# Kernel optimization log

Hardware: AMD Instinct MI355X
Metric: run time of the kernel (lower is better)

Reference implementation:

```python
import jax, jax.numpy as jnp
import numpy as np

B, N, IN, E, H, F = 64, 256, 128, 256, 8, 1024


def setup_inputs() -> dict:
    key = jax.random.key(0)
    ks = jax.random.split(key, 16)
    x = jax.random.normal(ks[0], (B, N, IN), jnp.float32)
    adj = (jax.random.uniform(ks[1], (B, N, N)) < 0.1).astype(jnp.float32)
    adj = jnp.maximum(adj, adj.transpose(0, 2, 1))  # symmetric 0/1 adjacency
    mask = jax.random.randint(ks[2], (B, N), 0, 2).astype(jnp.float32)
    dist = jax.random.normal(ks[3], (B, N, N), jnp.float32)

    def lin(k, i, o):
        return (jax.random.normal(k, (i, o), jnp.float32) / np.sqrt(i)).astype(jnp.float32)

    return dict(
        x=x, adj=adj, mask=mask, dist=dist,
        W1=lin(ks[4], IN, E), b1=jnp.zeros((E,), jnp.float32),
        W2=lin(ks[5], E, E), b2=jnp.zeros((E,), jnp.float32),
        W3=lin(ks[6], E, E), b3=jnp.zeros((E,), jnp.float32),
        ln1_g=jnp.ones((E,), jnp.float32), ln1_b=jnp.zeros((E,), jnp.float32),
        Wq=lin(ks[7], E, H * E), Wk=lin(ks[8], E, H * E), Wv=lin(ks[9], E, H * E),
        Wo=lin(ks[10], H * E, E), bo=jnp.zeros((E,), jnp.float32),
        ln2_g=jnp.ones((E,), jnp.float32), ln2_b=jnp.zeros((E,), jnp.float32),
        Wf1=lin(ks[11], E, F), bf1=jnp.zeros((F,), jnp.float32),
        Wf2=lin(ks[12], F, E), bf2=jnp.zeros((E,), jnp.float32),
    )


def _layernorm(x, g, b):
    m = x.mean(-1, keepdims=True)
    v = ((x - m) ** 2).mean(-1, keepdims=True)
    return (x - m) * jax.lax.rsqrt(v + 1e-5) * g + b


def reference(x, adj, mask, dist, W1, b1, W2, b2, W3, b3, ln1_g, ln1_b,
              Wq, Wk, Wv, Wo, bo, ln2_g, ln2_b, Wf1, bf1, Wf2, bf2):
    # --- DenseGCNConv normalization (add self-loops, sym-normalize) ---
    eye = jnp.eye(N, dtype=adj.dtype)
    A = adj * (1.0 - eye) + eye                      # fill_diag(adj, 1)
    dis = jax.lax.rsqrt(jnp.clip(A.sum(-1), 1.0, None))
    An = dis[:, :, None] * A * dis[:, None, :]       # D^-1/2 A D^-1/2, [B,N,N]
    m3 = mask[:, :, None]

    def gcn(h, W, b):
        return (jnp.einsum('bij,bjf->bif', An, h @ W) + b) * m3

    g1 = jax.nn.relu(gcn(x, W1, b1))
    g2 = jax.nn.relu(gcn(g1, W2, b2))
    g3 = jax.nn.relu(gcn(g2, W3, b3))
    gcn_res = g1 + g2 + g3

    # --- masked MHA with distance bias (head dim = E per head) ---
    h = _layernorm(gcn_res, ln1_g, ln1_b)
    mh = mask[:, None, :, None]                      # [B,1,N,1]
    q = (h @ Wq).reshape(B, N, H, E).transpose(0, 2, 1, 3) * mh
    k = (h @ Wk).reshape(B, N, H, E).transpose(0, 2, 1, 3) * mh
    v = (h @ Wv).reshape(B, N, H, E).transpose(0, 2, 1, 3) * mh
    a = jnp.einsum('bhne,bhme->bhnm', q * (E ** -0.5), k) + dist[:, None]
    am = (mask[:, :, None] * mask[:, None, :])[:, None]  # [B,1,N,N]
    a = jnp.where(am == 0, -1e9, a)
    a = jax.nn.softmax(a, axis=-1)
    a = jnp.where(am == 0, 0.0, a)
    y = jnp.einsum('bhnm,bhme->bhne', a, v).transpose(0, 2, 1, 3).reshape(B, N, H * E)
    y = (y @ Wo + bo) * m3
    att = gcn_res + y

    # --- FFN block ---
    f = _layernorm(att, ln2_g, ln2_b)
    f = (jax.nn.gelu(f @ Wf1 + bf1, approximate=False) @ Wf2 + bf2) * m3
    att = att + f
    return gcn_res + att
```

## Files before the change

### kernel.cpp

```cpp
#include <hip/hip_runtime.h>
#include <hip/hip_bf16.h>
#include <cmath>

#define BB 64
#define NNODES 256
#define INF_ 128
#define EE 256
#define HH 8
#define FFN 1024
#define BNROWS 16384

typedef __attribute__((ext_vector_type(8))) short short8;
typedef __attribute__((ext_vector_type(4))) float floatx4;
typedef __attribute__((ext_vector_type(4))) unsigned short ushort4v;

__device__ __forceinline__ float b2f(unsigned short u) {
  union { unsigned u32; float f; } w; w.u32 = ((unsigned)u) << 16; return w.f;
}
__device__ __forceinline__ unsigned short f2b(float f) {
  union { float f; unsigned u32; } w; w.f = f;
  unsigned r = w.u32 + 0x7FFFu + ((w.u32 >> 16) & 1u);
  return (unsigned short)(r >> 16);
}
__device__ __forceinline__ float gelu_f(float x) {
  const float z = 0.7978845608028654f * (x + 0.044715f * x * x * x);
  const float e = __expf(2.0f * z);
  const float th = (e - 1.0f) / (e + 1.0f);
  return 0.5f * x * (1.0f + th);
}

typedef const __attribute__((address_space(1))) void GV;
typedef __attribute__((address_space(3))) void LV;

__device__ __forceinline__ void gl_lds16(const unsigned short* g,
                                         unsigned short* l, int lane) {
#if __has_builtin(__builtin_amdgcn_global_load_lds)
  __builtin_amdgcn_global_load_lds((GV*)g, (LV*)l, 16, 0, 0);
#else
  *(short8*)(l + lane * 8) = *(const short8*)g;
#endif
}

struct PackArgs {
  const float* src[12];
  unsigned short* dst[12];
  int R[12], C[12];
  int start[13];
};

__launch_bounds__(256)
__global__ void pack_kernel(PackArgs a)
{
  __shared__ float tile[32][33];
  const int bid = blockIdx.x;
  int j = 0;
  while (bid >= a.start[j + 1]) j++;
  const int lb = bid - a.start[j];
  const float* src = a.src[j];
  unsigned short* dst = a.dst[j];
  const int R = a.R[j], C = a.C[j];

  if (C == 0) {
    const int i = (lb * 256 + threadIdx.x) * 4;
    if (i >= R) return;
    floatx4 v = *(const floatx4*)(src + i);
    ushort4v o;
    #pragma unroll
    for (int k = 0; k < 4; k++) o[k] = f2b(v[k]);
    *(ushort4v*)(dst + i) = o;
    return;
  }
  const int tpr = C >> 5;
  const int c0 = (lb % tpr) * 32, r0 = (lb / tpr) * 32;
  const int tx = threadIdx.x & 31, ty = threadIdx.x >> 5;
  #pragma unroll
  for (int i = ty; i < 32; i += 8)
    tile[i][tx] = src[(long long)(r0 + i) * C + c0 + tx];
  __syncthreads();
  #pragma unroll
  for (int i = ty; i < 32; i += 8)
    dst[(long long)(c0 + i) * R + r0 + tx] = f2b(tile[tx][i]);
}

__global__ void deg_kernel(const float* __restrict__ adj,
                           float* __restrict__ dis)
{
  const int g = blockIdx.x * 4 + (threadIdx.x >> 6);
  const int lane = threadIdx.x & 63;
  const int i = g & 255;
  floatx4 v = *(const floatx4*)(adj + (long long)g * 256 + lane * 4);
  float s = 0.f;
  #pragma unroll
  for (int jj = 0; jj < 4; jj++) {
    const int j = lane * 4 + jj;
    s += (j == i) ? 1.0f : v[jj];
  }
  #pragma unroll
  for (int off = 32; off > 0; off >>= 1) s += __shfl_xor(s, off);
  if (lane == 0) dis[g] = 1.0f / sqrtf(fmaxf(s, 1.0f));
}

__global__ void an_kernel(const float* __restrict__ adj,
                          const float* __restrict__ dis,
                          unsigned short* __restrict__ An)
{
  const long long base = ((long long)blockIdx.x * 256 + threadIdx.x) * 4;
  const int rowg = (int)(base >> 8);
  const int i = rowg & 255;
  const int brow = rowg & ~255;
  const int j0 = (int)(base & 255);
  const float di = dis[rowg];
  floatx4 v = *(const floatx4*)(adj + base);
  ushort4v o;
  #pragma unroll
  for (int jj = 0; jj < 4; jj++) {
    const int j = j0 + jj;
    const float a = (j == i) ? 1.0f : v[jj];
    o[jj] = f2b(di * dis[brow + j] * a);
  }
  *(ushort4v*)(An + base) = o;
}

__launch_bounds__(512, 4)
__global__ void gemm_kernel(const unsigned short* __restrict__ A, int lda,
                            long long sAo, long long sAi,
                            const unsigned short* __restrict__ Bm, int ldb,
                            long long sBo, long long sBi,
                            void* __restrict__ Cv, int ldc,
                            long long sCo, long long sCi,
                            int K, int zshift, int mode, int flag,
                            const float* __restrict__ aux1,
                            const float* __restrict__ mask,
                            float* __restrict__ gcn,
                            void* __restrict__ aux2)
{
  __shared__ __align__(16) unsigned short sA[16384];
  __shared__ __align__(16) unsigned short sB[16384];

  const int t = threadIdx.x;
  const int z = blockIdx.z;
  const int zi = z & ((1 << zshift) - 1);
  const int zb = z >> zshift;
  const int m0 = blockIdx.x * 128;
  const int n0 = blockIdx.y * 128;
  A  += zb * sAo + zi * sAi;
  Bm += zb * sBo + zi * sBi;
  const long long cbase = zb * sCo + zi * sCi;

  const int lane = t & 63;
  const int w = t >> 6;
  const int wm = w >> 2, wn = w & 3;
  const int lm = lane & 15, qd = lane >> 4;

  floatx4 acc[4][2] = {};

  const int sub = lane >> 4;
  const int qs  = lane & 15;
  const unsigned short* pA[4];
  const unsigned short* pB[4];
  #pragma unroll
  for (int i = 0; i < 4; i++) {
    const int d = w * 4 + i;
    const int r = d * 4 + sub;
    const int co = (qs ^ (r & 7)) * 8;
    pA[i] = A + (long long)(m0 + r) * lda + co;
    pB[i] = Bm + (long long)(n0 + r) * ldb + co;
  }

  for (int kk = 0; kk < K; kk += 128) {
    #pragma unroll
    for (int i = 0; i < 4; i++) {
      gl_lds16(pA[i] + kk, &sA[(w * 4 + i) * 512], lane);
      gl_lds16(pB[i] + kk, &sB[(w * 4 + i) * 512], lane);
    }
    __syncthreads();

    #pragma unroll
    for (int ks = 0; ks < 4; ks++) {
      short8 af[4], bg[2];
      const int q = ks * 4 + qd;
      #pragma unroll
      for (int mi = 0; mi < 4; mi++) {
        const int r = wm * 64 + mi * 16 + lm;
        af[mi] = *(const short8*)&sA[r * 128 + ((q ^ (r & 7)) * 8)];
      }
      #pragma unroll
      for (int ni = 0; ni < 2; ni++) {
        const int r = wn * 32 + ni * 16 + lm;
        bg[ni] = *(const short8*)&sB[r * 128 + ((q ^ (r & 7)) * 8)];
      }
      #pragma unroll
      for (int mi = 0; mi < 4; mi++)
        #pragma unroll
        for (int ni = 0; ni < 2; ni++)
          acc[mi][ni] = __builtin_amdgcn_mfma_f32_16x16x32_bf16(
              af[mi], bg[ni], acc[mi][ni], 0, 0, 0);
    }
    __syncthreads();
  }

  #pragma unroll
  for (int mi = 0; mi < 4; mi++) {
    const int row0 = m0 + wm * 64 + mi * 16 + qd * 4;
    #pragma unroll
    for (int ni = 0; ni < 2; ni++) {
      const int col = n0 + wn * 32 + ni * 16 + lm;
      floatx4 a = acc[mi][ni];
      if (mode == 0) {
        float* Cf = (float*)Cv;
        #pragma unroll
        for (int r = 0; r < 4; r++)
          Cf[cbase + (long long)(row0 + r) * ldc + col] = a[r];
      } else if (mode == 1) {
        unsigned short* Cb = (unsigned short*)Cv;
        #pragma unroll
        for (int r = 0; r < 4; r++)
          Cb[cbase + (long long)(row0 + r) * ldc + col] = f2b(a[r]);
      } else if (mode == 2) {
        float* Cf = (float*)Cv;
        #pragma unroll
        for (int r = 0; r < 4; r++)
          Cf[cbase + (long long)(row0 + r) * ldc + col] += a[r];
      } else if (mode == 3) {
        unsigned short* Cb = (unsigned short*)Cv;
        const float bv = aux1[col];
        #pragma unroll
        for (int r = 0; r < 4; r++)
          Cb[cbase + (long long)(row0 + r) * ldc + col] = f2b(gelu_f(a[r] + bv));
      } else if (mode == 5) {
        const int b = row0 >> 8, n = row0 & 255;
        ushort4v o;
        #pragma unroll
        for (int r = 0; r < 4; r++) o[r] = f2b(a[r]);
        *(ushort4v*)((unsigned short*)Cv + (long long)b * 65536 + col * 256 + n) = o;
      } else if (mode == 8) {
        float* Cf = (float*)Cv;
        const float* attf = (const float*)aux2;
        const float bv = aux1[col];
        #pragma unroll
        for (int r = 0; r < 4; r++) {
          const long long idx = (long long)(row0 + r) * 256 + col;
          Cf[idx] = gcn[idx] + attf[idx] + (a[r] + bv) * mask[row0 + r];
        }
      } else if (mode == 9) {
        const int token = zb * 256 + col;
        const float m = mask[token];
        ushort4v o; floatx4 g;
        #pragma unroll
        for (int r = 0; r < 4; r++) {
          const float v = fmaxf((a[r] + aux1[row0 + r]) * m, 0.f);
          o[r] = f2b(v); g[r] = v;
        }
        *(ushort4v*)((unsigned short*)Cv + (long long)token * 256 + row0) = o;
        float* gp = gcn + (long long)token * 256 + row0;
        if (flag) { floatx4 old = *(const floatx4*)gp; g += old; }
        *(floatx4*)gp = g;
      } else if (mode == 12) {
        float* Cf = (float*)Cv;
        const float bv = aux1[col];
        #pragma unroll
        for (int r = 0; r < 4; r++) {
          const long long idx = (long long)(row0 + r) * 256 + col;
          Cf[idx] = gcn[idx] + (a[r] + bv) * mask[row0 + r];
        }
      } else if (mode == 13) {
        unsigned short* Cb = (unsigned short*)Cv;
        #pragma unroll
        for (int r = 0; r < 4; r++)
          Cb[cbase + (long long)(row0 + r) * ldc + col] = f2b(a[r] * 0.0625f);
      } else {
        if (col < 2048) {
          unsigned short* Cb = (unsigned short*)Cv;
          #pragma unroll
          for (int r = 0; r < 4; r++)
            Cb[(long long)(row0 + r) * 2048 + col] = f2b(a[r]);
        } else {
          const int z2 = (row0 >> 8) * 8 + ((col >> 8) - 8);
          const int e = col & 255, n = row0 & 255;
          ushort4v o;
          #pragma unroll
          for (int r = 0; r < 4; r++) o[r] = f2b(a[r]);
          *(ushort4v*)((unsigned short*)aux2 + (long long)z2 * 65536 + e * 256 + n) = o;
        }
      }
    }
  }
}

__launch_bounds__(512, 4)
__global__ void attn_kernel(unsigned short* __restrict__ QP,
                            const unsigned short* __restrict__ HBF,
                            const unsigned short* __restrict__ VT,
                            const unsigned short* __restrict__ DSTB,
                            const float* __restrict__ mask)
{
  __shared__ __align__(16) unsigned short sP[16896];
  __shared__ __align__(16) unsigned short sKV[16384];
  __shared__ float redm[4][64];
  __shared__ float reds[4][64];

  const int bi = blockIdx.x;
  const int x = bi & 7;
  const int h = (bi >> 3) & 7;
  const int p = (bi >> 6) * 8 + x;
  const int b = p >> 2, mt = p & 3;
  const int m0 = mt * 64;
  const int z = b * 8 + h;

  const int t = threadIdx.x, lane = t & 63, w = t >> 6;
  const int lm = lane & 15, qd = lane >> 4;
  const int wm2 = w >> 2, wn4 = w & 3;

  unsigned short* Qm = QP + ((long long)(b * 256 + m0)) * 2048 + h * 256;
  const unsigned short* Hb = HBF + (long long)b * 65536;
  const unsigned short* Vb = VT + (long long)z * 65536;
  const unsigned short* db = DSTB + (long long)b * 65536 + (long long)m0 * 256;
  const float* maskb = mask + b * 256;

  const int rin2 = lane >> 5, qs32 = lane & 31;
  const int rin8 = lane >> 3, qs8  = lane & 7;

  floatx4 S[2][4];
  #pragma unroll
  for (int mi = 0; mi < 2; mi++)
    #pragma unroll
    for (int ni = 0; ni < 4; ni++) {
      const int col = wn4 * 64 + ni * 16 + lm;
      #pragma unroll
      for (int r = 0; r < 4; r++) {
        const int row = wm2 * 32 + mi * 16 + qd * 4 + r;
        S[mi][ni][r] = b2f(db[row * 256 + col]);
      }
    }

  #pragma unroll
  for (int i = 0; i < 4; i++) {
    const int d = w * 4 + i;
    const int r = d * 2 + rin2;
    gl_lds16(Qm + (long long)r * 2048 + ((qs32 ^ (r & 7)) * 8), &sP[d * 512], lane);
  }
  #pragma unroll
  for (int i = 0; i < 4; i++) {
    const int d = w * 4 + i;
    const int r = d * 8 + rin8;
    gl_lds16(Hb + (long long)r * 256 + ((qs8 ^ (r & 7)) * 8), &sKV[d * 512], lane);
  }
  __syncthreads();

  for (int c = 0; c < 4; c++) {
    __builtin_amdgcn_s_setprio(1);
    #pragma unroll
    for (int ks = 0; ks < 2; ks++) {
      const int ol = ks * 4 + qd;
      short8 af[2], bg[4];
      #pragma unroll
      for (int mi = 0; mi < 2; mi++) {
        const int r = wm2 * 32 + mi * 16 + lm;
        const int q = c * 8 + ol;
        af[mi] = *(const short8*)&sP[r * 256 + ((q ^ (r & 7)) * 8)];
      }
      #pragma unroll
      for (int ni = 0; ni < 4; ni++) {
        const int kk = wn4 * 64 + ni * 16 + lm;
        bg[ni] = *(const short8*)&sKV[kk * 64 + ((ol ^ (kk & 7)) * 8)];
      }
      #pragma unroll
      for (int mi = 0; mi < 2; mi++)
        #pragma unroll
        for (int ni = 0; ni < 4; ni++)
          S[mi][ni] = __builtin_amdgcn_mfma_f32_16x16x32_bf16(
              af[mi], bg[ni], S[mi][ni], 0, 0, 0);
    }
    __builtin_amdgcn_s_setprio(0);
    __syncthreads();
    if (c < 3) {
      #pragma unroll
      for (int i = 0; i < 4; i++) {
        const int d = w * 4 + i;
        const int r = d * 8 + rin8;
        gl_lds16(Hb + (long long)r * 256 + (c + 1) * 64 + ((qs8 ^ (r & 7)) * 8),
                 &sKV[d * 512], lane);
      }
      __syncthreads();
    }
  }

  #pragma unroll
  for (int i = 0; i < 4; i++) {
    const int d = w * 4 + i;
    const int r = d * 8 + rin8;
    gl_lds16(Vb + (long long)r * 256 + ((qs8 ^ (r & 7)) * 8), &sKV[d * 512], lane);
  }

  float mkv[4];
  #pragma unroll
  for (int ni = 0; ni < 4; ni++) mkv[ni] = maskb[wn4 * 64 + ni * 16 + lm];

  float lred[2][4];
  #pragma unroll
  for (int mi = 0; mi < 2; mi++) {
    #pragma unroll
    for (int r = 0; r < 4; r++) {
      const int row = wm2 * 32 + mi * 16 + qd * 4 + r;
      const float mq = maskb[m0 + row];
      float mx = -3e38f;
      #pragma unroll
      for (int ni = 0; ni < 4; ni++) {
        const float v = (mq != 0.f && mkv[ni] != 0.f) ? S[mi][ni][r] : -1e9f;
        S[mi][ni][r] = v;
        mx = fmaxf(mx, v);
      }
      lred[mi][r] = mx;
    }
  }
  #pragma unroll
  for (int off = 1; off < 16; off <<= 1)
    #pragma unroll
    for (int mi = 0; mi < 2; mi++)
      #pragma unroll
      for (int r = 0; r < 4; r++)
        lred[mi][r] = fmaxf(lred[mi][r], __shfl_xor(lred[mi][r], off));
  if (lm == 0)
    #pragma unroll
    for (int mi = 0; mi < 2; mi++)
      #pragma unroll
      for (int r = 0; r < 4; r++)
        redm[wn4][wm2 * 32 + mi * 16 + qd * 4 + r] = lred[mi][r];
  __syncthreads();

  #pragma unroll
  for (int mi = 0; mi < 2; mi++) {
    #pragma unroll
    for (int r = 0; r < 4; r++) {
      const int row = wm2 * 32 + mi * 16 + qd * 4 + r;
      const float gmax = fmaxf(fmaxf(redm[0][row], redm[1][row]),
                               fmaxf(redm[2][row], redm[3][row]));
      float ss = 0.f;
      #pragma unroll
      for (int ni = 0; ni < 4; ni++) {
        const float e = __expf(S[mi][ni][r] - gmax);
        S[mi][ni][r] = e;
        ss += e;
      }
      lred[mi][r] = ss;
    }
  }
  #pragma unroll
  for (int off = 1; off < 16; off <<= 1)
    #pragma unroll
    for (int mi = 0; mi < 2; mi++)
      #pragma unroll
      for (int r = 0; r < 4; r++)
        lred[mi][r] += __shfl_xor(lred[mi][r], off);
  if (lm == 0)
    #pragma unroll
    for (int mi = 0; mi < 2; mi++)
      #pragma unroll
      for (int r = 0; r < 4; r++)
        reds[wn4][wm2 * 32 + mi * 16 + qd * 4 + r] = lred[mi][r];
  __syncthreads();

  #pragma unroll
  for (int mi = 0; mi < 2; mi++)
    #pragma unroll
    for (int r = 0; r < 4; r++) {
      const int row = wm2 * 32 + mi * 16 + qd * 4 + r;
      const float inv = 1.0f / (reds[0][row] + reds[1][row] +
                                reds[2][row] + reds[3][row]);
      #pragma unroll
      for (int ni = 0; ni < 4; ni++) {
        const int kl = ni * 16 + lm;
        const int slot = (kl >> 3) ^ (row & 7);
        sP[wn4 * 4096 + row * 64 + slot * 8 + (kl & 7)] =
            f2b(S[mi][ni][r] * inv);
      }
    }
  __syncthreads();

  floatx4 Y[2][4] = {};
  for (int c = 0; c < 4; c++) {
    __builtin_amdgcn_s_setprio(1);
    #pragma unroll
    for (int ks = 0; ks < 2; ks++) {
      const int ol = ks * 4 + qd;
      short8 af[2], bg[4];
      #pragma unroll
      for (int mi = 0; mi < 2; mi++) {
        const int r = wm2 * 32 + mi * 16 + lm;
        af[mi] = *(const short8*)&sP[c * 4096 + r * 64 + ((ol ^ (r & 7)) * 8)];
      }
      #pragma unroll
      for (int ni = 0; ni < 4; ni++) {
        const int ee = wn4 * 64 + ni * 16 + lm;
        bg[ni] = *(const short8*)&sKV[ee * 64 + ((ol ^ (ee & 7)) * 8)];
      }
      #pragma unroll
      for (int mi = 0; mi < 2; mi++)
        #pragma unroll
        for (int ni = 0; ni < 4; ni++)
          Y[mi][ni] = __builtin_amdgcn_mfma_f32_16x16x32_bf16(
              af[mi], bg[ni], Y[mi][ni], 0, 0, 0);
    }
    __builtin_amdgcn_s_setprio(0);
    __syncthreads();
    if (c < 3) {
      #pragma unroll
      for (int i = 0; i < 4; i++) {
        const int d = w * 4 + i;
        const int r = d * 8 + rin8;
        gl_lds16(Vb + (long long)r * 256 + (c + 1) * 64 + ((qs8 ^ (r & 7)) * 8),
                 &sKV[d * 512], lane);
      }
      __syncthreads();
    }
  }

  #pragma unroll
  for (int mi = 0; mi < 2; mi++)
    #pragma unroll
    for (int ni = 0; ni < 4; ni++) {
      const int col = wn4 * 64 + ni * 16 + lm;
      #pragma unroll
      for (int r = 0; r < 4; r++) {
        const int rl = wm2 * 32 + mi * 16 + qd * 4 + r;
        sP[rl * 264 + col] = f2b(Y[mi][ni][r]);
      }
    }
  __syncthreads();
  #pragma unroll
  for (int it = 0; it < 4; it++) {
    const int idx = it * 512 + t;
    const int row = idx >> 5, u = idx & 31;
    short8 v = *(const short8*)&sP[row * 264 + u * 8];
    *(short8*)(Qm + (long long)row * 2048 + u * 8) = v;
  }
}

__global__ void ln_kernel(const float* __restrict__ X,
                          const float* __restrict__ gam,
                          const float* __restrict__ bet,
                          unsigned short* __restrict__ out)
{
  const int g = blockIdx.x * 4 + (threadIdx.x >> 6);
  const int lane = threadIdx.x & 63;
  floatx4 v = *(const floatx4*)(X + (long long)g * 256 + lane * 4);
  float s = v[0] + v[1] + v[2] + v[3];
  float sq = v[0]*v[0] + v[1]*v[1] + v[2]*v[2] + v[3]*v[3];
  #pragma unroll
  for (int off = 32; off > 0; off >>= 1) {
    s  += __shfl_xor(s, off);
    sq += __shfl_xor(sq, off);
  }
  const float mean = s * (1.0f / 256.0f);
  const float var = sq * (1.0f / 256.0f) - mean * mean;
  const float rs = 1.0f / sqrtf(var + 1e-5f);
  ushort4v o;
  #pragma unroll
  for (int jj = 0; jj < 4; jj++) {
    const int c = lane * 4 + jj;
    o[jj] = f2b((v[jj] - mean) * rs * gam[c] + bet[c]);
  }
  *(ushort4v*)(out + (long long)g * 256 + lane * 4) = o;
}

static inline void launch_gemm(hipStream_t st, int M, int N, int batch,
    const void* A, int lda, long long sAo, long long sAi,
    const void* B, int ldb, long long sBo, long long sBi,
    void* C, int ldc, long long sCo, long long sCi,
    int K, int zshift, int mode, int flag,
    const float* aux1, const float* mask, float* gcn, void* aux2)
{
  dim3 grid(M / 128, N / 128, batch), blk(512);
  gemm_kernel<<<grid, blk, 0, st>>>(
      (const unsigned short*)A, lda, sAo, sAi,
      (const unsigned short*)B, ldb, sBo, sBi,
      C, ldc, sCo, sCi, K, zshift, mode, flag, aux1, mask, gcn, aux2);
}

extern "C" void kernel_launch(void* const* d_in, const int* in_sizes, int n_in,
                              void* d_out, int out_size, void* d_ws, size_t ws_size,
                              hipStream_t stream)
{
  (void)in_sizes; (void)n_in; (void)out_size;
  const float* x    = (const float*)d_in[0];
  const float* adj  = (const float*)d_in[1];
  const float* mask = (const float*)d_in[2];
  const float* dist = (const float*)d_in[3];
  const float* W1   = (const float*)d_in[4];
  const float* b1   = (const float*)d_in[5];
  const float* W2   = (const float*)d_in[6];
  const float* b2   = (const float*)d_in[7];
  const float* W3   = (const float*)d_in[8];
  const float* b3   = (const float*)d_in[9];
  const float* ln1g = (const float*)d_in[10];
  const float* ln1b = (const float*)d_in[11];
  const float* Wq   = (const float*)d_in[12];
  const float* Wk   = (const float*)d_in[13];
  const float* Wv   = (const float*)d_in[14];
  const float* Wo   = (const float*)d_in[15];
  const float* bo   = (const float*)d_in[16];
  const float* ln2g = (const float*)d_in[17];
  const float* ln2b = (const float*)d_in[18];
  const float* Wf1  = (const float*)d_in[19];
  const float* bf1  = (const float*)d_in[20];
  const float* Wf2  = (const float*)d_in[21];
  const float* bf2  = (const float*)d_in[22];

  char* w = (char*)d_ws;
  auto alloc = [&](size_t sz) { void* p = (void*)w; w += sz; return p; };
  unsigned short* W1T   = (unsigned short*)alloc(65536);
  unsigned short* W2T   = (unsigned short*)alloc(131072);
  unsigned short* W3T   = (unsigned short*)alloc(131072);
  unsigned short* ABH   = (unsigned short*)alloc(1048576);
  unsigned short* WVT   = (unsigned short*)alloc(1048576);
  unsigned short* WOT   = (unsigned short*)alloc(1048576);
  unsigned short* WF1T  = (unsigned short*)alloc(524288);
  unsigned short* WF2T  = (unsigned short*)alloc(524288);
  unsigned short* WQb   = (unsigned short*)alloc(1048576);
  unsigned short* WKb   = (unsigned short*)alloc(1048576);
  unsigned short* XBF   = (unsigned short*)alloc(4194304);
  unsigned short* DSTB  = (unsigned short*)alloc(8388608);
  float*          GCN   = (float*)         alloc(16777216);
  float*          U     = (float*)         alloc(16777216);
  unsigned short* HBF   = (unsigned short*)alloc(8388608);
  float*          DIS   = (float*)         alloc(65536);
  char* scratch = (char*)alloc(134217728);
  if ((size_t)(w - (char*)d_ws) > ws_size) return;
  unsigned short* AN  = (unsigned short*)scratch;
  unsigned short* TT  = (unsigned short*)(scratch + 8388608);
  unsigned short* GBF = (unsigned short*)(scratch + 16777216);
  unsigned short* QPB = (unsigned short*)scratch;
  unsigned short* VT  = (unsigned short*)(scratch + 67108864);
  unsigned short* FFB = (unsigned short*)scratch;

  PackArgs pa;
  const float* srcs[11] = {W1, W2, W3, Wv, Wo, Wf1, Wf2, x, Wq, Wk, dist};
  unsigned short* dsts[11] = {W1T, W2T, W3T, WVT, WOT, WF1T, WF2T, XBF, WQb, WKb, DSTB};
  const int Rs[11] = {128, 256, 256, 256, 2048, 256, 1024,
                      BNROWS * INF_, EE * HH * EE, EE * HH * EE, BB * 65536};
  const int Cs[11] = {256, 256, 256, 2048, 256, 1024, 256, 0, 0, 0, 0};
  const int sts[12] = {0, 32, 96, 160, 672, 1184, 1440, 1696, 3744, 4256, 4768, 8864};
  for (int j = 0; j < 11; j++) {
    pa.src[j] = srcs[j]; pa.dst[j] = dsts[j]; pa.R[j] = Rs[j]; pa.C[j] = Cs[j];
  }
  for (int j = 0; j < 12; j++) pa.start[j] = sts[j];
  pack_kernel<<<8864, 256, 0, stream>>>(pa);

  deg_kernel<<<4096, 256, 0, stream>>>(adj, DIS);
  an_kernel<<<4096, 256, 0, stream>>>(adj, DIS, AN);

  launch_gemm(stream, 256, 256, 8, WKb, 2048, 256, 0, WQb, 2048, 256, 0,
              ABH, 256, 65536, 0, 256, 0, 13, 0, nullptr, nullptr, nullptr, nullptr);

  launch_gemm(stream, BNROWS, EE, 1, XBF, 128, 0,0, W1T, 128, 0,0,
              TT, 256, 0,0, 128, 0, 5, 0, nullptr, nullptr, nullptr, nullptr);
  launch_gemm(stream, 256, 256, BB, TT, 256, 65536,0, AN, 256, 65536,0,
              GBF, 256, 0,0, 256, 0, 9, 0, b1, mask, GCN, nullptr);
  launch_gemm(stream, BNROWS, EE, 1, GBF, 256, 0,0, W2T, 256, 0,0,
              TT, 256, 0,0, 256, 0, 5, 0, nullptr, nullptr, nullptr, nullptr);
  launch_gemm(stream, 256, 256, BB, TT, 256, 65536,0, AN, 256, 65536,0,
              GBF, 256, 0,0, 256, 0, 9, 1, b2, mask, GCN, nullptr);
  launch_gemm(stream, BNROWS, EE, 1, GBF, 256, 0,0, W3T, 256, 0,0,
              TT, 256, 0,0, 256, 0, 5, 0, nullptr, nullptr, nullptr, nullptr);
  launch_gemm(stream, 256, 256, BB, TT, 256, 65536,0, AN, 256, 65536,0,
              GBF, 256, 0,0, 256, 0, 9, 1, b3, mask, GCN, nullptr);

  ln_kernel<<<4096, 256, 0, stream>>>(GCN, ln1g, ln1b, HBF);

  launch_gemm(stream, BNROWS, 4096, 1, HBF, 256, 0,0, ABH, 256, 0,0,
              QPB, 2048, 0,0, 256, 0, 15, 0, nullptr, nullptr, nullptr, VT);
  attn_kernel<<<2048, 512, 0, stream>>>(QPB, HBF, VT, DSTB, mask);
  launch_gemm(stream, BNROWS, EE, 1, QPB, 2048, 0,0, WOT, 2048, 0,0,
              U, 256, 0,0, 2048, 0, 12, 0, bo, mask, GCN, nullptr);

  ln_kernel<<<4096, 256, 0, stream>>>(U, ln2g, ln2b, HBF);
  launch_gemm(stream, BNROWS, FFN, 1, HBF, 256, 0,0, WF1T, 256, 0,0,
              FFB, 1024, 0,0, 256, 0, 3, 0, bf1, nullptr, nullptr, nullptr);
  launch_gemm(stream, BNROWS, EE, 1, FFB, 1024, 0,0, WF2T, 1024, 0,0,
              d_out, 256, 0,0, 1024, 0, 8, 0, bf2, mask, GCN, U);
}
```

Baseline: 467.4 us.

## Fuse query projection into attention kernel and double-buffer K/V staging

The separate GEMM that produced the projected queries (h·Wq·Wk^T folded into ABH) is removed. The projection is now computed inside the attention kernel from the layer-normed rows, so the pre-attention GEMM only produces V (N halves from 4096 to 2048 columns). The attention kernel gains a unified double-buffered staging pipeline using explicit vmcnt waits and raw barriers in place of __syncthreads. The aim is to avoid writing and re-reading the large projected-query buffer and to overlap global-to-LDS loads with MFMA work. In exchange, each block recomputes its 64x256x256 projection and relies on hand-managed wait counts.

```diff
diff --git a/kernel.cpp b/kernel.cpp
--- a/kernel.cpp
+++ b/kernel.cpp
@@ -40,6 +40,13 @@
   *(short8*)(l + lane * 8) = *(const short8*)g;
 #endif
 }
+
+#define VMW2() asm volatile("s_waitcnt vmcnt(2)" ::: "memory")
+#define VMW0() asm volatile("s_waitcnt vmcnt(0)" ::: "memory")
+#define LGW0() asm volatile("s_waitcnt lgkmcnt(0)" ::: "memory")
+#define MBAR() do { asm volatile("" ::: "memory"); \
+                    __builtin_amdgcn_s_barrier(); \
+                    asm volatile("" ::: "memory"); } while (0)
 
 struct PackArgs {
   const float* src[12];
@@ -269,19 +276,12 @@
         for (int r = 0; r < 4; r++)
           Cb[cbase + (long long)(row0 + r) * ldc + col] = f2b(a[r] * 0.0625f);
       } else {
-        if (col < 2048) {
-          unsigned short* Cb = (unsigned short*)Cv;
-          #pragma unroll
-          for (int r = 0; r < 4; r++)
-            Cb[(long long)(row0 + r) * 2048 + col] = f2b(a[r]);
-        } else {
-          const int z2 = (row0 >> 8) * 8 + ((col >> 8) - 8);
-          const int e = col & 255, n = row0 & 255;
-          ushort4v o;
-          #pragma unroll
-          for (int r = 0; r < 4; r++) o[r] = f2b(a[r]);
-          *(ushort4v*)((unsigned short*)aux2 + (long long)z2 * 65536 + e * 256 + n) = o;
-        }
+        const int z2 = (row0 >> 8) * 8 + (col >> 8);
+        const int e = col & 255, n = row0 & 255;
+        ushort4v o;
+        #pragma unroll
+        for (int r = 0; r < 4; r++) o[r] = f2b(a[r]);
+        *(ushort4v*)((unsigned short*)aux2 + (long long)z2 * 65536 + e * 256 + n) = o;
       }
     }
   }
@@ -290,12 +290,13 @@
 __launch_bounds__(512, 4)
 __global__ void attn_kernel(unsigned short* __restrict__ QP,
                             const unsigned short* __restrict__ HBF,
+                            const unsigned short* __restrict__ ABH,
                             const unsigned short* __restrict__ VT,
                             const unsigned short* __restrict__ DSTB,
                             const float* __restrict__ mask)
 {
-  __shared__ __align__(16) unsigned short sP[16896];
-  __shared__ __align__(16) unsigned short sKV[16384];
+  __shared__ __align__(16) unsigned short sR0[16896];
+  __shared__ __align__(16) unsigned short sS[16384];
   __shared__ float redm[4][64];
   __shared__ float reds[4][64];
 
@@ -311,15 +312,14 @@
   const int lm = lane & 15, qd = lane >> 4;
   const int wm2 = w >> 2, wn4 = w & 3;
 
-  unsigned short* Qm = QP + ((long long)(b * 256 + m0)) * 2048 + h * 256;
+  unsigned short* Ym = QP + ((long long)(b * 256 + m0)) * 2048 + h * 256;
   const unsigned short* Hb = HBF + (long long)b * 65536;
+  const unsigned short* Hq = Hb + (long long)m0 * 256;
+  const unsigned short* Ah = ABH + (long long)h * 65536;
   const unsigned short* Vb = VT + (long long)z * 65536;
   const unsigned short* db = DSTB + (long long)b * 65536 + (long long)m0 * 256;
   const float* maskb = mask + b * 256;
 
-  const int rin2 = lane >> 5, qs32 = lane & 31;
-  const int rin8 = lane >> 3, qs8  = lane & 7;
-
   floatx4 S[2][4];
   #pragma unroll
   for (int mi = 0; mi < 2; mi++)
@@ -333,63 +333,111 @@
       }
     }
 
-  #pragma unroll
-  for (int i = 0; i < 4; i++) {
-    const int d = w * 4 + i;
-    const int r = d * 2 + rin2;
-    gl_lds16(Qm + (long long)r * 2048 + ((qs32 ^ (r & 7)) * 8), &sP[d * 512], lane);
-  }
-  #pragma unroll
-  for (int i = 0; i < 4; i++) {
-    const int d = w * 4 + i;
-    const int r = d * 8 + rin8;
-    gl_lds16(Hb + (long long)r * 256 + ((qs8 ^ (r & 7)) * 8), &sKV[d * 512], lane);
-  }
-  __syncthreads();
-
-  for (int c = 0; c < 4; c++) {
+  int eoff0, eoff1;
+  {
+    const int rA = lane >> 2, sl = lane & 3;
+    const int r0 = (w * 2 + 0) * 16 + rA;
+    const int r1 = (w * 2 + 1) * 16 + rA;
+    eoff0 = r0 * 256 + ((sl ^ ((r0 >> 1) & 3)) * 8);
+    eoff1 = r1 * 256 + ((sl ^ ((r1 >> 1) & 3)) * 8);
+  }
+  const int ld0 = (w * 2 + 0) * 512;
+  const int ld1 = (w * 2 + 1) * 512;
+
+  auto STAGE = [&](int c) {
+    const unsigned short* bp =
+        (c < 8 ? Ah : (c < 16 ? Hb : Vb)) + (c & 7) * 32;
+    const int bb = (c & 1) * 8192;
+    gl_lds16(bp + eoff0, &sS[bb + ld0], lane);
+    gl_lds16(bp + eoff1, &sS[bb + ld1], lane);
+  };
+
+  {
+    const int rin2 = lane >> 5, qs32 = lane & 31;
+    #pragma unroll
+    for (int i = 0; i < 4; i++) {
+      const int d = w * 4 + i;
+      const int r = d * 2 + rin2;
+      gl_lds16(Hq + (long long)r * 256 + ((qs32 ^ (r & 7)) * 8),
+               &sR0[d * 512], lane);
+    }
+  }
+  STAGE(0); STAGE(1);
+  VMW2();
+  MBAR();
+
+  floatx4 accq[2][4] = {};
+  #pragma unroll
+  for (int c = 0; c < 8; c++) {
     __builtin_amdgcn_s_setprio(1);
-    #pragma unroll
-    for (int ks = 0; ks < 2; ks++) {
-      const int ol = ks * 4 + qd;
-      short8 af[2], bg[4];
-      #pragma unroll
-      for (int mi = 0; mi < 2; mi++) {
-        const int r = wm2 * 32 + mi * 16 + lm;
-        const int q = c * 8 + ol;
-        af[mi] = *(const short8*)&sP[r * 256 + ((q ^ (r & 7)) * 8)];
-      }
+    short8 af[2], bg[4];
+    #pragma unroll
+    for (int mi = 0; mi < 2; mi++) {
+      const int r = wm2 * 32 + mi * 16 + lm;
+      const int q = c * 4 + qd;
+      af[mi] = *(const short8*)&sR0[r * 256 + ((q ^ (r & 7)) * 8)];
+    }
+    const int bb = (c & 1) * 8192;
+    #pragma unroll
+    for (int ni = 0; ni < 4; ni++) {
+      const int rr = wn4 * 64 + ni * 16 + lm;
+      bg[ni] = *(const short8*)&sS[bb + rr * 32 + ((qd ^ ((rr >> 1) & 3)) * 8)];
+    }
+    #pragma unroll
+    for (int mi = 0; mi < 2; mi++)
+      #pragma unroll
+      for (int ni = 0; ni < 4; ni++)
+        accq[mi][ni] = __builtin_amdgcn_mfma_f32_16x16x32_bf16(
+            af[mi], bg[ni], accq[mi][ni], 0, 0, 0);
+    __builtin_amdgcn_s_setprio(0);
+    MBAR();
+    STAGE(c + 2);
+    VMW2();
+    MBAR();
+  }
+
+  #pragma unroll
+  for (int mi = 0; mi < 2; mi++)
+    #pragma unroll
+    for (int rr = 0; rr < 4; rr++) {
+      const int row = wm2 * 32 + mi * 16 + qd * 4 + rr;
       #pragma unroll
       for (int ni = 0; ni < 4; ni++) {
-        const int kk = wn4 * 64 + ni * 16 + lm;
-        bg[ni] = *(const short8*)&sKV[kk * 64 + ((ol ^ (kk & 7)) * 8)];
-      }
-      #pragma unroll
-      for (int mi = 0; mi < 2; mi++)
-        #pragma unroll
-        for (int ni = 0; ni < 4; ni++)
-          S[mi][ni] = __builtin_amdgcn_mfma_f32_16x16x32_bf16(
-              af[mi], bg[ni], S[mi][ni], 0, 0, 0);
-    }
+        const int col = wn4 * 64 + ni * 16 + lm;
+        const int o = col >> 3;
+        sR0[row * 256 + ((o ^ (row & 7)) * 8) + (col & 7)] = f2b(accq[mi][ni][rr]);
+      }
+    }
+  LGW0();
+  MBAR();
+
+  #pragma unroll
+  for (int c = 8; c < 16; c++) {
+    __builtin_amdgcn_s_setprio(1);
+    short8 af[2], bg[4];
+    #pragma unroll
+    for (int mi = 0; mi < 2; mi++) {
+      const int r = wm2 * 32 + mi * 16 + lm;
+      const int q = (c - 8) * 4 + qd;
+      af[mi] = *(const short8*)&sR0[r * 256 + ((q ^ (r & 7)) * 8)];
+    }
+    const int bb = (c & 1) * 8192;
+    #pragma unroll
+    for (int ni = 0; ni < 4; ni++) {
+      const int rr = wn4 * 64 + ni * 16 + lm;
+      bg[ni] = *(const short8*)&sS[bb + rr * 32 + ((qd ^ ((rr >> 1) & 3)) * 8)];
+    }
+    #pragma unroll
+    for (int mi = 0; mi < 2; mi++)
+      #pragma unroll
+      for (int ni = 0; ni < 4; ni++)
+        S[mi][ni] = __builtin_amdgcn_mfma_f32_16x16x32_bf16(
+            af[mi], bg[ni], S[mi][ni], 0, 0, 0);
     __builtin_amdgcn_s_setprio(0);
-    __syncthreads();
-    if (c < 3) {
-      #pragma unroll
-      for (int i = 0; i < 4; i++) {
-        const int d = w * 4 + i;
-        const int r = d * 8 + rin8;
-        gl_lds16(Hb + (long long)r * 256 + (c + 1) * 64 + ((qs8 ^ (r & 7)) * 8),
-                 &sKV[d * 512], lane);
-      }
-      __syncthreads();
-    }
-  }
-
-  #pragma unroll
-  for (int i = 0; i < 4; i++) {
-    const int d = w * 4 + i;
-    const int r = d * 8 + rin8;
-    gl_lds16(Vb + (long long)r * 256 + ((qs8 ^ (r & 7)) * 8), &sKV[d * 512], lane);
+    MBAR();
+    STAGE(c + 2);
+    VMW2();
+    MBAR();
   }
 
   float mkv[4];
@@ -426,7 +474,8 @@
       #pragma unroll
       for (int r = 0; r < 4; r++)
         redm[wn4][wm2 * 32 + mi * 16 + qd * 4 + r] = lred[mi][r];
-  __syncthreads();
+  LGW0();
+  MBAR();
 
   #pragma unroll
   for (int mi = 0; mi < 2; mi++) {
@@ -458,7 +507,8 @@
       #pragma unroll
       for (int r = 0; r < 4; r++)
         reds[wn4][wm2 * 32 + mi * 16 + qd * 4 + r] = lred[mi][r];
-  __syncthreads();
+  LGW0();
+  MBAR();
 
   #pragma unroll
   for (int mi = 0; mi < 2; mi++)
@@ -471,47 +521,46 @@
       for (int ni = 0; ni < 4; ni++) {
         const int kl = ni * 16 + lm;
         const int slot = (kl >> 3) ^ (row & 7);
-        sP[wn4 * 4096 + row * 64 + slot * 8 + (kl & 7)] =
+        sR0[wn4 * 4096 + row * 64 + slot * 8 + (kl & 7)] =
             f2b(S[mi][ni][r] * inv);
       }
     }
-  __syncthreads();
+  LGW0();
+  MBAR();
 
   floatx4 Y[2][4] = {};
-  for (int c = 0; c < 4; c++) {
+  #pragma unroll
+  for (int c = 16; c < 24; c++) {
     __builtin_amdgcn_s_setprio(1);
-    #pragma unroll
-    for (int ks = 0; ks < 2; ks++) {
-      const int ol = ks * 4 + qd;
-      short8 af[2], bg[4];
-      #pragma unroll
-      for (int mi = 0; mi < 2; mi++) {
-        const int r = wm2 * 32 + mi * 16 + lm;
-        af[mi] = *(const short8*)&sP[c * 4096 + r * 64 + ((ol ^ (r & 7)) * 8)];
-      }
-      #pragma unroll
-      for (int ni = 0; ni < 4; ni++) {
-        const int ee = wn4 * 64 + ni * 16 + lm;
-        bg[ni] = *(const short8*)&sKV[ee * 64 + ((ol ^ (ee & 7)) * 8)];
-      }
-      #pragma unroll
-      for (int mi = 0; mi < 2; mi++)
-        #pragma unroll
-        for (int ni = 0; ni < 4; ni++)
-          Y[mi][ni] = __builtin_amdgcn_mfma_f32_16x16x32_bf16(
-              af[mi], bg[ni], Y[mi][ni], 0, 0, 0);
-    }
+    const int pp = (c - 16) >> 1;
+    const int op = ((c - 16) & 1) * 4 + qd;
+    short8 af[2], bg[4];
+    #pragma unroll
+    for (int mi = 0; mi < 2; mi++) {
+      const int r = wm2 * 32 + mi * 16 + lm;
+      af[mi] = *(const short8*)&sR0[pp * 4096 + r * 64 + ((op ^ (r & 7)) * 8)];
+    }
+    const int bb = (c & 1) * 8192;
+    #pragma unroll
+    for (int ni = 0; ni < 4; ni++) {
+      const int rr = wn4 * 64 + ni * 16 + lm;
+      bg[ni] = *(const short8*)&sS[bb + rr * 32 + ((qd ^ ((rr >> 1) & 3)) * 8)];
+    }
+    #pragma unroll
+    for (int mi = 0; mi < 2; mi++)
+      #pragma unroll
+      for (int ni = 0; ni < 4; ni++)
+        Y[mi][ni] = __builtin_amdgcn_mfma_f32_16x16x32_bf16(
+            af[mi], bg[ni], Y[mi][ni], 0, 0, 0);
     __builtin_amdgcn_s_setprio(0);
-    __syncthreads();
-    if (c < 3) {
-      #pragma unroll
-      for (int i = 0; i < 4; i++) {
-        const int d = w * 4 + i;
-        const int r = d * 8 + rin8;
-        gl_lds16(Vb + (long long)r * 256 + (c + 1) * 64 + ((qs8 ^ (r & 7)) * 8),
-                 &sKV[d * 512], lane);
-      }
-      __syncthreads();
+    MBAR();
+    if (c < 22) {
+      STAGE(c + 2);
+      VMW2();
+      MBAR();
+    } else if (c == 22) {
+      VMW0();
+      MBAR();
     }
   }
 
@@ -523,16 +572,17 @@
       #pragma unroll
       for (int r = 0; r < 4; r++) {
         const int rl = wm2 * 32 + mi * 16 + qd * 4 + r;
-        sP[rl * 264 + col] = f2b(Y[mi][ni][r]);
-      }
-    }
-  __syncthreads();
+        sR0[rl * 264 + col] = f2b(Y[mi][ni][r]);
+      }
+    }
+  LGW0();
+  MBAR();
   #pragma unroll
   for (int it = 0; it < 4; it++) {
     const int idx = it * 512 + t;
     const int row = idx >> 5, u = idx & 31;
-    short8 v = *(const short8*)&sP[row * 264 + u * 8];
-    *(short8*)(Qm + (long long)row * 2048 + u * 8) = v;
+    short8 v = *(const short8*)&sR0[row * 264 + u * 8];
+    *(short8*)(Ym + (long long)row * 2048 + u * 8) = v;
   }
 }
 
@@ -667,9 +717,9 @@
 
   ln_kernel<<<4096, 256, 0, stream>>>(GCN, ln1g, ln1b, HBF);
 
-  launch_gemm(stream, BNROWS, 4096, 1, HBF, 256, 0,0, ABH, 256, 0,0,
-              QPB, 2048, 0,0, 256, 0, 15, 0, nullptr, nullptr, nullptr, VT);
-  attn_kernel<<<2048, 512, 0, stream>>>(QPB, HBF, VT, DSTB, mask);
+  launch_gemm(stream, BNROWS, 2048, 1, HBF, 256, 0,0, WVT, 256, 0,0,
+              QPB, 2048, 0,0, 256, 0, 16, 0, nullptr, nullptr, nullptr, VT);
+  attn_kernel<<<2048, 512, 0, stream>>>(QPB, HBF, ABH, VT, DSTB, mask);
   launch_gemm(stream, BNROWS, EE, 1, QPB, 2048, 0,0, WOT, 2048, 0,0,
               U, 256, 0,0, 2048, 0, 12, 0, bo, mask, GCN, nullptr);
 
```

Result: no change. 464.9 us (-0.5%).
